# Performance work log

Measured on AMD Instinct MI355X. Metric: run time of the kernel, lower is better.

The kernel has to match this reference:

```python
import jax, jax.numpy as jnp
import numpy as np

B, S, DIM, H = 1, 4096, 1024, 16
HEAD_DIM = DIM // H
ROPE_THETA = 10000.0
LN_EPS = 1e-5


def _rope_cos_sin(seq_len, dim, theta):
    # frequencies over the FULL model dim (rope applied before head split, as in source)
    inv_freq = 1.0 / (theta ** (jnp.arange(0, dim, 2, dtype=jnp.float32) / dim))  # (dim/2,)
    ang = jnp.arange(seq_len, dtype=jnp.float32)[:, None] * inv_freq[None, :]     # (S, dim/2)
    cos = jnp.concatenate([jnp.cos(ang), jnp.cos(ang)], axis=-1)                  # (S, dim)
    sin = jnp.concatenate([jnp.sin(ang), jnp.sin(ang)], axis=-1)
    return cos, sin


def _rotate_half(x):
    d = x.shape[-1] // 2
    return jnp.concatenate([-x[..., d:], x[..., :d]], axis=-1)


def _apply_rope(x, cos, sin):
    # x: (B, S, dim); cos/sin: (S, dim)
    return x * cos[None] + _rotate_half(x) * sin[None]


def setup_inputs() -> dict:
    key = jax.random.key(0)
    ks = jax.random.split(key, 5)
    sc = 1.0 / np.sqrt(DIM)
    return {
        "x": jax.random.normal(ks[0], (B, S, DIM), dtype=jnp.float32),
        "Wqkv": jax.random.normal(ks[1], (DIM, 3 * DIM), dtype=jnp.float32) * sc,
        "bqkv": jax.random.normal(ks[2], (3 * DIM,), dtype=jnp.float32) * 0.01,
        "Wo": jax.random.normal(ks[3], (DIM, DIM), dtype=jnp.float32) * sc,
        "bo": jax.random.normal(ks[4], (DIM,), dtype=jnp.float32) * 0.01,
        "gamma": jnp.ones((DIM,), dtype=jnp.float32),
        "beta": jnp.zeros((DIM,), dtype=jnp.float32),
    }


def reference(x, Wqkv, bqkv, Wo, bo, gamma, beta):
    b, s, d = x.shape
    qkv = x @ Wqkv + bqkv                      # (B, S, 3*dim)
    q, k, v = jnp.split(qkv, 3, axis=-1)       # each (B, S, dim)
    cos, sin = _rope_cos_sin(s, d, ROPE_THETA)
    q = _apply_rope(q, cos, sin)
    k = _apply_rope(k, cos, sin)
    # split heads
    q = q.reshape(b, s, H, HEAD_DIM)
    k = k.reshape(b, s, H, HEAD_DIM)
    v = v.reshape(b, s, H, HEAD_DIM)
    scale = 1.0 / np.sqrt(HEAD_DIM)
    scores = jnp.einsum('bqhd,bkhd->bhqk', q, k) * scale  # (B, H, S, S)
    causal = jnp.triu(jnp.ones((s, s), dtype=bool), k=1)
    scores = jnp.where(causal[None, None], -jnp.inf, scores)
    attn = jax.nn.softmax(scores, axis=-1)
    out = jnp.einsum('bhqk,bkhd->bqhd', attn, v).reshape(b, s, d)
    out = out @ Wo + bo
    # LayerNorm (dropout is identity in eval mode)
    mu = jnp.mean(out, axis=-1, keepdims=True)
    var = jnp.mean(jnp.square(out - mu), axis=-1, keepdims=True)
    return (out - mu) * jax.lax.rsqrt(var + LN_EPS) * gamma + beta
```

## Files before the change

kernel.cpp:

```cpp
#include <hip/hip_runtime.h>
#include <cstdint>
#include <cstddef>

#define S_LEN 4096
#define DIM   1024
#define NH    16
#define HD    64
#define QKV_N 3072

typedef __attribute__((ext_vector_type(8))) short short8;
typedef __attribute__((ext_vector_type(4))) float f32x4;
typedef __attribute__((ext_vector_type(4))) unsigned short ushort4v;
typedef __attribute__((ext_vector_type(2))) unsigned int uint2v;

__device__ inline unsigned short f2bf(float x) {
    unsigned int u = __builtin_bit_cast(unsigned int, x);
    u += 0x7fffu + ((u >> 16) & 1u);
    return (unsigned short)(u >> 16);
}
__device__ inline float bf2f(unsigned short u) {
    return __builtin_bit_cast(float, (unsigned int)u << 16);
}
__device__ inline unsigned int pack2_bf16_rh(float lo, float hi) {
    unsigned int a = __builtin_bit_cast(unsigned int, lo) + 0x8000u;
    unsigned int b = __builtin_bit_cast(unsigned int, hi) + 0x8000u;
    return __builtin_amdgcn_perm(b, a, 0x07060302u);
}

__device__ inline void gl_lds16(const void* g, void* l) {
    __builtin_amdgcn_global_load_lds(
        (const __attribute__((address_space(1))) void*)g,
        (__attribute__((address_space(3))) void*)l, 16, 0, 0);
}

template <bool BF16OUT>
__global__ __launch_bounds__(256) void gemm_mfma_kernel(
    const unsigned short* __restrict__ A,
    const unsigned short* __restrict__ Bt,
    const float* __restrict__ bias,
    void* __restrict__ Cv,
    int M, int N, int K)
{
    __shared__ unsigned short As[128 * 32];
    __shared__ unsigned short Bs[128 * 32];

    const int t    = threadIdx.x;
    const int w    = t >> 6;
    const int lane = t & 63;
    const int ln   = lane & 15;
    const int quad = lane >> 4;
    const int bm   = blockIdx.y * 128;
    const int bn   = blockIdx.x * 128;
    const int wm   = (w & 1) * 64;
    const int wn   = (w >> 1) * 64;

    f32x4 acc[4][4];
#pragma unroll
    for (int i = 0; i < 4; ++i)
#pragma unroll
        for (int j = 0; j < 4; ++j) acc[i][j] = (f32x4){0.f, 0.f, 0.f, 0.f};

    const int lr = lane >> 2;
    const int lc = (lane & 3) * 8;
    const unsigned short* ga = A  + (size_t)(bm + w * 32 + lr) * K + lc;
    const unsigned short* gb = Bt + (size_t)(bn + w * 32 + lr) * K + lc;
    unsigned short* la = &As[(w * 32) * 32];
    unsigned short* lb = &Bs[(w * 32) * 32];

    for (int k0 = 0; k0 < K; k0 += 32) {
        gl_lds16(ga,            la);
        gl_lds16(ga + 16 * K,   la + 16 * 32);
        gl_lds16(gb,            lb);
        gl_lds16(gb + 16 * K,   lb + 16 * 32);
        ga += 32; gb += 32;
        __syncthreads();

        short8 af[4], bf[4];
#pragma unroll
        for (int i = 0; i < 4; ++i)
            af[i] = *(const short8*)&As[(wm + i * 16 + ln) * 32 + quad * 8];
#pragma unroll
        for (int j = 0; j < 4; ++j)
            bf[j] = *(const short8*)&Bs[(wn + j * 16 + ln) * 32 + quad * 8];
#pragma unroll
        for (int i = 0; i < 4; ++i)
#pragma unroll
            for (int j = 0; j < 4; ++j)
                acc[i][j] = __builtin_amdgcn_mfma_f32_16x16x32_bf16(af[i], bf[j], acc[i][j], 0, 0, 0);
        __syncthreads();
    }

#pragma unroll
    for (int j = 0; j < 4; ++j) {
        const int col = bn + wn + j * 16 + ln;
        const float bv = bias[col];
#pragma unroll
        for (int i = 0; i < 4; ++i) {
            const int row0 = bm + wm + i * 16 + quad * 4;
#pragma unroll
            for (int r = 0; r < 4; ++r) {
                const float v = acc[i][j][r] + bv;
                if (BF16OUT)
                    ((unsigned short*)Cv)[(size_t)(row0 + r) * N + col] = f2bf(v);
                else
                    ((float*)Cv)[(size_t)(row0 + r) * N + col] = v;
            }
        }
    }
}

__global__ __launch_bounds__(256) void prep1_kernel(
    const float* __restrict__ x, unsigned short* __restrict__ xb,
    const float* __restrict__ Wqkv, unsigned short* __restrict__ WqkvT,
    const float* __restrict__ Wo, unsigned short* __restrict__ WoT)
{
    __shared__ unsigned short L[64][72];
    const int b = blockIdx.x;
    const int t = threadIdx.x;

    if (b < 2048) {
        const size_t i = ((size_t)b * 256 + t) * 8;
        float4 a = *(const float4*)(x + i);
        float4 c = *(const float4*)(x + i + 4);
        short8 p = { (short)f2bf(a.x), (short)f2bf(a.y), (short)f2bf(a.z), (short)f2bf(a.w),
                     (short)f2bf(c.x), (short)f2bf(c.y), (short)f2bf(c.z), (short)f2bf(c.w) };
        *(short8*)(xb + i) = p;
        return;
    }
    const float* W;
    unsigned short* Wt;
    int N, n0, k0;
    if (b < 2816) {
        const int wb = b - 2048;
        W = Wqkv; Wt = WqkvT; N = QKV_N;
        n0 = (wb % 48) * 64; k0 = (wb / 48) * 64;
    } else {
        const int wb = b - 2816;
        W = Wo; Wt = WoT; N = DIM;
        n0 = (wb & 15) * 64; k0 = (wb >> 4) * 64;
    }
    const int kr = t >> 2, cb = (t & 3) * 16;
    const float* wp = W + (size_t)(k0 + kr) * N + n0 + cb;
#pragma unroll
    for (int u = 0; u < 16; u += 4) {
        float4 v = *(const float4*)(wp + u);
        ushort4v p = { f2bf(v.x), f2bf(v.y), f2bf(v.z), f2bf(v.w) };
        *(ushort4v*)&L[kr][cb + u] = p;
    }
    __syncthreads();
    const int nr = t >> 2, kb = (t & 3) * 16;
    short8 lo, hi;
#pragma unroll
    for (int u = 0; u < 8; ++u) lo[u] = (short)L[kb + u][nr];
#pragma unroll
    for (int u = 0; u < 8; ++u) hi[u] = (short)L[kb + 8 + u][nr];
    unsigned short* op = Wt + (size_t)(n0 + nr) * 1024 + k0 + kb;
    *(short8*)op       = lo;
    *(short8*)(op + 8) = hi;
}

__global__ __launch_bounds__(256) void prep2_kernel(
    const unsigned short* __restrict__ qkvb,
    unsigned short* __restrict__ Qb,
    unsigned short* __restrict__ Kb,
    unsigned short* __restrict__ Vt)
{
    __shared__ unsigned short L[64][72];
    const int b = blockIdx.x;
    const int t = threadIdx.x;

    if (b < 2048) {
        const int idx = b * 256 + t;
        const int j   = (idx & 127) * 4;
        const int s   = idx >> 7;
        const unsigned short* row = qkvb + (size_t)s * QKV_N;
        unsigned short* qo = Qb + (size_t)s * DIM;
        unsigned short* ko = Kb + (size_t)s * DIM;
        const float sf = (float)s;
        const float QSCALE = 0.18033688011112042f;
        const float C1 = -0.025952563241307517f;
        const float INV2PI = 0.15915494309189535f;

        float cs[4], sn[4];
#pragma unroll
        for (int e = 0; e < 4; ++e) {
            const float invf2pi = exp2f((float)(j + e) * C1) * INV2PI;
            float rev = sf * invf2pi;
            rev -= floorf(rev);
            sn[e] = __builtin_amdgcn_sinf(rev);
            cs[e] = __builtin_amdgcn_cosf(rev);
        }
        ushort4v q1 = *(const ushort4v*)(row + j);
        ushort4v q2 = *(const ushort4v*)(row + 512 + j);
        ushort4v k1 = *(const ushort4v*)(row + DIM + j);
        ushort4v k2 = *(const ushort4v*)(row + DIM + 512 + j);
        ushort4v qa, qb4, ka, kb4;
#pragma unroll
        for (int e = 0; e < 4; ++e) {
            const float x1 = bf2f(q1[e]), x2 = bf2f(q2[e]);
            const float y1 = bf2f(k1[e]), y2 = bf2f(k2[e]);
            qa[e]  = f2bf((x1 * cs[e] - x2 * sn[e]) * QSCALE);
            qb4[e] = f2bf((x2 * cs[e] + x1 * sn[e]) * QSCALE);
            ka[e]  = f2bf(y1 * cs[e] - y2 * sn[e]);
            kb4[e] = f2bf(y2 * cs[e] + y1 * sn[e]);
        }
        *(ushort4v*)(qo + j)       = qa;
        *(ushort4v*)(qo + 512 + j) = qb4;
        *(ushort4v*)(ko + j)       = ka;
        *(ushort4v*)(ko + 512 + j) = kb4;
        return;
    }

    const int vb = b - 2048;
    const int c0 = (vb & 15) * 64;
    const int bs = (vb >> 4) * 64;
    const int sl = t >> 2, cb = (t & 3) * 16;
    const unsigned short* vp = qkvb + (size_t)(bs + sl) * QKV_N + 2 * DIM + c0 + cb;
    *(short8*)&L[sl][cb]     = *(const short8*)vp;
    *(short8*)&L[sl][cb + 8] = *(const short8*)(vp + 8);
    __syncthreads();
    const int cl = t >> 2, sb = (t & 3) * 16;
    short8 lo, hi;
#pragma unroll
    for (int u = 0; u < 8; ++u) lo[u] = (short)L[sb + u][cl];
#pragma unroll
    for (int u = 0; u < 8; ++u) hi[u] = (short)L[sb + 8 + u][cl];
    unsigned short* op = Vt + (size_t)(c0 + cl) * S_LEN + bs + sb;
    *(short8*)op       = lo;
    *(short8*)(op + 8) = hi;
}

__global__ __launch_bounds__(256) void attn_mfma_kernel(
    const unsigned short* __restrict__ Qb,
    const unsigned short* __restrict__ Kb,
    const unsigned short* __restrict__ Vt,
    float* __restrict__ Op,
    float* __restrict__ lp)
{
    __shared__ unsigned short Ks[64][72];
    __shared__ unsigned short Vs[64][72];
    __shared__ unsigned short Ps[4][16][72];

    const int t    = threadIdx.x;
    const int w    = t >> 6;
    const int lane = t & 63;
    const int ln   = lane & 15;
    const int quad = lane >> 4;
    const int p    = blockIdx.x;
    const int half = blockIdx.y;
    const int h    = blockIdx.z;

    const int sc_ = t >> 2;
    const int so  = (t & 3) * 16;

#pragma unroll
    for (int phase = 0; phase < 2; ++phase) {
        const int qt  = phase == 0 ? (63 - p) : p;
        const int q0  = qt * 64;
        const int nkt = qt + 1;
        const int c0  = (nkt + 1) >> 1;
        const int kt_begin = half == 0 ? 0 : c0;
        const int kt_end   = half == 0 ? c0 : nkt;

        short8 qf[2];
        {
            const unsigned short* qp = Qb + (size_t)(q0 + w * 16 + ln) * DIM + h * HD + quad * 8;
            qf[0] = *(const short8*)qp;
            qf[1] = *(const short8*)(qp + 32);
        }

        f32x4 o[4];
#pragma unroll
        for (int db = 0; db < 4; ++db) o[db] = (f32x4){0.f, 0.f, 0.f, 0.f};
        float lrow = 0.f;

        short8 kr0, kr1, vr0, vr1;
        {
            const int k0 = kt_begin * 64;
            const unsigned short* kp = Kb + (size_t)(k0 + sc_) * DIM + h * HD + so;
            kr0 = *(const short8*)kp;  kr1 = *(const short8*)(kp + 8);
            const unsigned short* vp = Vt + (size_t)(h * HD + sc_) * S_LEN + k0 + so;
            vr0 = *(const short8*)vp;  vr1 = *(const short8*)(vp + 8);
        }

        for (int kt = kt_begin; kt < kt_end; ++kt) {
            __syncthreads();
            *(short8*)&Ks[sc_][so]     = kr0;
            *(short8*)&Ks[sc_][so + 8] = kr1;
            *(short8*)&Vs[sc_][so]     = vr0;
            *(short8*)&Vs[sc_][so + 8] = vr1;
            if (kt + 1 < kt_end) {
                const int k1 = (kt + 1) * 64;
                const unsigned short* kp = Kb + (size_t)(k1 + sc_) * DIM + h * HD + so;
                kr0 = *(const short8*)kp;  kr1 = *(const short8*)(kp + 8);
                const unsigned short* vp = Vt + (size_t)(h * HD + sc_) * S_LEN + k1 + so;
                vr0 = *(const short8*)vp;  vr1 = *(const short8*)(vp + 8);
            }
            __syncthreads();

            f32x4 sc[4];
#pragma unroll
            for (int kb = 0; kb < 4; ++kb) sc[kb] = (f32x4){0.f, 0.f, 0.f, 0.f};
#pragma unroll
            for (int kk = 0; kk < 2; ++kk) {
#pragma unroll
                for (int kb = 0; kb < 4; ++kb) {
                    short8 kf = *(const short8*)&Ks[kb * 16 + ln][kk * 32 + quad * 8];
                    sc[kb] = __builtin_amdgcn_mfma_f32_16x16x32_bf16(kf, qf[kk], sc[kb], 0, 0, 0);
                }
            }

            if (kt == nkt - 1) {
                const int qg = w * 16 + ln;
                const int kb0 = kt * 64 - q0;
#pragma unroll
                for (int kb = 0; kb < 4; ++kb) {
                    const int key = kb0 + kb * 16 + quad * 4;
#pragma unroll
                    for (int r = 0; r < 4; ++r)
                        if (key + r > qg) sc[kb][r] = -1e30f;
                }
            }

            float psp[4];
#pragma unroll
            for (int kb = 0; kb < 4; ++kb) {
                float pv[4];
#pragma unroll
                for (int r = 0; r < 4; ++r) pv[r] = exp2f(sc[kb][r]);
                psp[kb] = (pv[0] + pv[1]) + (pv[2] + pv[3]);
                uint2v pk = { pack2_bf16_rh(pv[0], pv[1]), pack2_bf16_rh(pv[2], pv[3]) };
                *(uint2v*)&Ps[w][ln][kb * 16 + quad * 4] = pk;
            }
            float ps = (psp[0] + psp[1]) + (psp[2] + psp[3]);
            ps += __shfl_xor(ps, 16);
            ps += __shfl_xor(ps, 32);
            lrow += ps;

#pragma unroll
            for (int kk = 0; kk < 2; ++kk) {
                short8 pf = *(const short8*)&Ps[w][ln][kk * 32 + quad * 8];
#pragma unroll
                for (int db = 0; db < 4; ++db) {
                    short8 vf = *(const short8*)&Vs[db * 16 + ln][kk * 32 + quad * 8];
                    o[db] = __builtin_amdgcn_mfma_f32_16x16x32_bf16(vf, pf, o[db], 0, 0, 0);
                }
            }
        }

        {
            float* op = Op + ((size_t)half * S_LEN + q0 + w * 16 + ln) * DIM + h * HD + quad * 4;
#pragma unroll
            for (int db = 0; db < 4; ++db)
                *(f32x4*)(op + db * 16) = o[db];
            if (quad == 0)
                lp[((size_t)half * NH + h) * S_LEN + q0 + w * 16 + ln] = lrow;
        }
    }
}

__global__ __launch_bounds__(256) void combine_kernel(
    const float* __restrict__ Op, const float* __restrict__ lp,
    unsigned short* __restrict__ attnb)
{
    const int row = blockIdx.x;
    const int t   = threadIdx.x;
    const int d   = t * 4;
    const int h   = t >> 4;
    f32x4 a = *(const f32x4*)&Op[(size_t)row * DIM + d];
    f32x4 b = *(const f32x4*)&Op[((size_t)S_LEN + row) * DIM + d];
    const float l = lp[(size_t)h * S_LEN + row] + lp[((size_t)NH + h) * S_LEN + row];
    const float inv = 1.0f / l;
    ushort4v o;
#pragma unroll
    for (int e = 0; e < 4; ++e) o[e] = f2bf((a[e] + b[e]) * inv);
    *(ushort4v*)&attnb[(size_t)row * DIM + d] = o;
}

__global__ __launch_bounds__(256) void ln_kernel(
    const float* __restrict__ in, const float* __restrict__ gamma,
    const float* __restrict__ beta, float* __restrict__ out)
{
    const int row = blockIdx.x;
    const int t = threadIdx.x;
    const float4 v = *(const float4*)&in[(size_t)row * DIM + t * 4];
    float s  = v.x + v.y + v.z + v.w;
    float sq = v.x * v.x + v.y * v.y + v.z * v.z + v.w * v.w;
#pragma unroll
    for (int off = 1; off < 64; off <<= 1) {
        s  += __shfl_xor(s, off);
        sq += __shfl_xor(sq, off);
    }
    __shared__ float red[8];
    const int wv = t >> 6, ln = t & 63;
    if (ln == 0) { red[wv] = s; red[4 + wv] = sq; }
    __syncthreads();
    s  = red[0] + red[1] + red[2] + red[3];
    sq = red[4] + red[5] + red[6] + red[7];
    const float mu  = s * (1.0f / DIM);
    const float var = sq * (1.0f / DIM) - mu * mu;
    const float rs  = rsqrtf(var + 1e-5f);
    const float4 g = *(const float4*)&gamma[t * 4];
    const float4 b = *(const float4*)&beta[t * 4];
    float4 o = { (v.x - mu) * rs * g.x + b.x,
                 (v.y - mu) * rs * g.y + b.y,
                 (v.z - mu) * rs * g.z + b.z,
                 (v.w - mu) * rs * g.w + b.w };
    *(float4*)&out[(size_t)row * DIM + t * 4] = o;
}

extern "C" void kernel_launch(void* const* d_in, const int* in_sizes, int n_in,
                              void* d_out, int out_size, void* d_ws, size_t ws_size,
                              hipStream_t stream)
{
    const float* x     = (const float*)d_in[0];
    const float* Wqkv  = (const float*)d_in[1];
    const float* bqkv  = (const float*)d_in[2];
    const float* Wo    = (const float*)d_in[3];
    const float* bo    = (const float*)d_in[4];
    const float* gamma = (const float*)d_in[5];
    const float* beta  = (const float*)d_in[6];
    float* out = (float*)d_out;

    char* base = (char*)d_ws;
    unsigned short* qkvb  = (unsigned short*)base;
    unsigned short* attnb = (unsigned short*)base;
    float* Op   = (float*)(base + (size_t)8 * 1024 * 1024);
    float* proj = (float*)(base + (size_t)8 * 1024 * 1024);
    float* lp   = (float*)(base + (size_t)40 * 1024 * 1024);
    unsigned short* Qb    = (unsigned short*)(base + (size_t)48 * 1024 * 1024);
    unsigned short* Kb    = (unsigned short*)(base + (size_t)56 * 1024 * 1024);
    unsigned short* Vt    = (unsigned short*)(base + (size_t)64 * 1024 * 1024);
    unsigned short* xb    = (unsigned short*)(base + (size_t)72 * 1024 * 1024);
    unsigned short* WqkvT = (unsigned short*)(base + (size_t)80 * 1024 * 1024);
    unsigned short* WoT   = (unsigned short*)(base + (size_t)86 * 1024 * 1024);

    prep1_kernel<<<3072, 256, 0, stream>>>(x, xb, Wqkv, WqkvT, Wo, WoT);

    gemm_mfma_kernel<true><<<dim3(QKV_N / 128, S_LEN / 128), 256, 0, stream>>>(
        xb, WqkvT, bqkv, qkvb, S_LEN, QKV_N, DIM);

    prep2_kernel<<<3072, 256, 0, stream>>>(qkvb, Qb, Kb, Vt);

    attn_mfma_kernel<<<dim3(32, 2, NH), 256, 0, stream>>>(Qb, Kb, Vt, Op, lp);

    combine_kernel<<<S_LEN, 256, 0, stream>>>(Op, lp, attnb);

    gemm_mfma_kernel<false><<<dim3(DIM / 128, S_LEN / 128), 256, 0, stream>>>(
        attnb, WoT, bo, proj, S_LEN, DIM, DIM);

    ln_kernel<<<S_LEN, 256, 0, stream>>>(proj, gamma, beta, out);
}
```

Measured before the change: 259.9 us.

## Rework attention to 32x32 MFMA tiles with register-resident P and swizzled LDS

The attention kernel moves from 16x16x32 to 32x32x16 bf16 MFMA, with each wave owning 32 query rows, so a block now covers 128 queries and the grid halves. The softmax probabilities stay in registers and are rearranged with v_permlane32_swap instead of a round trip through shared memory. K and V tiles are double-buffered in XOR-swizzled LDS, which drops one barrier per iteration and avoids bank conflicts. The trade-offs are higher register pressure, fewer blocks to balance the causal work, and a wider causal-mask region spanning two key tiles.

```diff
diff --git a/kernel.cpp b/kernel.cpp
--- a/kernel.cpp
+++ b/kernel.cpp
@@ -10,8 +10,10 @@
 
 typedef __attribute__((ext_vector_type(8))) short short8;
 typedef __attribute__((ext_vector_type(4))) float f32x4;
+typedef __attribute__((ext_vector_type(16))) float f32x16;
 typedef __attribute__((ext_vector_type(4))) unsigned short ushort4v;
 typedef __attribute__((ext_vector_type(2))) unsigned int uint2v;
+typedef __attribute__((ext_vector_type(4))) unsigned int uint4v;
 
 __device__ inline unsigned short f2bf(float x) {
     unsigned int u = __builtin_bit_cast(unsigned int, x);
@@ -237,124 +239,144 @@
     float* __restrict__ Op,
     float* __restrict__ lp)
 {
-    __shared__ unsigned short Ks[64][72];
-    __shared__ unsigned short Vs[64][72];
-    __shared__ unsigned short Ps[4][16][72];
+    __shared__ unsigned short Ks[2][64 * 64];
+    __shared__ unsigned short Vs[2][64 * 64];
 
     const int t    = threadIdx.x;
     const int w    = t >> 6;
     const int lane = t & 63;
-    const int ln   = lane & 15;
-    const int quad = lane >> 4;
+    const int r31  = lane & 31;
+    const int hi   = lane >> 5;
     const int p    = blockIdx.x;
     const int half = blockIdx.y;
     const int h    = blockIdx.z;
 
-    const int sc_ = t >> 2;
-    const int so  = (t & 3) * 16;
+    const int srow  = t >> 2;
+    const int sch   = (t & 3) * 2;
+    const int ssw   = srow & 7;
+    const int soff0 = srow * 64 + ((sch ^ ssw) << 3);
+    const int soff1 = srow * 64 + (((sch + 1) ^ ssw) << 3);
+
+    const int rA = r31 * 64;
+    const int sw = r31 & 7;
 
 #pragma unroll
     for (int phase = 0; phase < 2; ++phase) {
-        const int qt  = phase == 0 ? (63 - p) : p;
-        const int q0  = qt * 64;
-        const int nkt = qt + 1;
-        const int c0  = (nkt + 1) >> 1;
+        const int qt  = phase == 0 ? (31 - p) : p;
+        const int q0  = qt * 128;
+        const int nkt = 2 * qt + 2;
+        const int c0  = nkt >> 1;
         const int kt_begin = half == 0 ? 0 : c0;
         const int kt_end   = half == 0 ? c0 : nkt;
 
-        short8 qf[2];
+        short8 qf[4];
         {
-            const unsigned short* qp = Qb + (size_t)(q0 + w * 16 + ln) * DIM + h * HD + quad * 8;
-            qf[0] = *(const short8*)qp;
-            qf[1] = *(const short8*)(qp + 32);
-        }
-
-        f32x4 o[4];
-#pragma unroll
-        for (int db = 0; db < 4; ++db) o[db] = (f32x4){0.f, 0.f, 0.f, 0.f};
+            const unsigned short* qp = Qb + (size_t)(q0 + w * 32 + r31) * DIM + h * HD + hi * 8;
+#pragma unroll
+            for (int kk = 0; kk < 4; ++kk) qf[kk] = *(const short8*)(qp + kk * 16);
+        }
+
+        f32x16 o0 = {}, o1 = {};
         float lrow = 0.f;
 
         short8 kr0, kr1, vr0, vr1;
         {
             const int k0 = kt_begin * 64;
-            const unsigned short* kp = Kb + (size_t)(k0 + sc_) * DIM + h * HD + so;
+            const unsigned short* kp = Kb + (size_t)(k0 + srow) * DIM + h * HD + sch * 8;
             kr0 = *(const short8*)kp;  kr1 = *(const short8*)(kp + 8);
-            const unsigned short* vp = Vt + (size_t)(h * HD + sc_) * S_LEN + k0 + so;
+            const unsigned short* vp = Vt + (size_t)(h * HD + srow) * S_LEN + k0 + sch * 8;
             vr0 = *(const short8*)vp;  vr1 = *(const short8*)(vp + 8);
         }
+        __syncthreads();
 
         for (int kt = kt_begin; kt < kt_end; ++kt) {
-            __syncthreads();
-            *(short8*)&Ks[sc_][so]     = kr0;
-            *(short8*)&Ks[sc_][so + 8] = kr1;
-            *(short8*)&Vs[sc_][so]     = vr0;
-            *(short8*)&Vs[sc_][so + 8] = vr1;
+            const int buf = (kt - kt_begin) & 1;
+            unsigned short* ks = &Ks[buf][0];
+            unsigned short* vs = &Vs[buf][0];
+            *(short8*)&ks[soff0] = kr0;
+            *(short8*)&ks[soff1] = kr1;
+            *(short8*)&vs[soff0] = vr0;
+            *(short8*)&vs[soff1] = vr1;
             if (kt + 1 < kt_end) {
                 const int k1 = (kt + 1) * 64;
-                const unsigned short* kp = Kb + (size_t)(k1 + sc_) * DIM + h * HD + so;
+                const unsigned short* kp = Kb + (size_t)(k1 + srow) * DIM + h * HD + sch * 8;
                 kr0 = *(const short8*)kp;  kr1 = *(const short8*)(kp + 8);
-                const unsigned short* vp = Vt + (size_t)(h * HD + sc_) * S_LEN + k1 + so;
+                const unsigned short* vp = Vt + (size_t)(h * HD + srow) * S_LEN + k1 + sch * 8;
                 vr0 = *(const short8*)vp;  vr1 = *(const short8*)(vp + 8);
             }
             __syncthreads();
 
-            f32x4 sc[4];
-#pragma unroll
-            for (int kb = 0; kb < 4; ++kb) sc[kb] = (f32x4){0.f, 0.f, 0.f, 0.f};
-#pragma unroll
-            for (int kk = 0; kk < 2; ++kk) {
-#pragma unroll
-                for (int kb = 0; kb < 4; ++kb) {
-                    short8 kf = *(const short8*)&Ks[kb * 16 + ln][kk * 32 + quad * 8];
-                    sc[kb] = __builtin_amdgcn_mfma_f32_16x16x32_bf16(kf, qf[kk], sc[kb], 0, 0, 0);
-                }
-            }
-
-            if (kt == nkt - 1) {
-                const int qg = w * 16 + ln;
-                const int kb0 = kt * 64 - q0;
-#pragma unroll
-                for (int kb = 0; kb < 4; ++kb) {
-                    const int key = kb0 + kb * 16 + quad * 4;
-#pragma unroll
-                    for (int r = 0; r < 4; ++r)
-                        if (key + r > qg) sc[kb][r] = -1e30f;
-                }
-            }
-
-            float psp[4];
-#pragma unroll
-            for (int kb = 0; kb < 4; ++kb) {
-                float pv[4];
-#pragma unroll
-                for (int r = 0; r < 4; ++r) pv[r] = exp2f(sc[kb][r]);
-                psp[kb] = (pv[0] + pv[1]) + (pv[2] + pv[3]);
-                uint2v pk = { pack2_bf16_rh(pv[0], pv[1]), pack2_bf16_rh(pv[2], pv[3]) };
-                *(uint2v*)&Ps[w][ln][kb * 16 + quad * 4] = pk;
-            }
-            float ps = (psp[0] + psp[1]) + (psp[2] + psp[3]);
-            ps += __shfl_xor(ps, 16);
+            f32x16 s0 = {}, s1 = {};
+#pragma unroll
+            for (int kk = 0; kk < 4; ++kk) {
+                const int co = (((kk * 2 + hi) ^ sw) << 3);
+                short8 kf0 = *(const short8*)&ks[rA + co];
+                short8 kf1 = *(const short8*)&ks[rA + 2048 + co];
+                s0 = __builtin_amdgcn_mfma_f32_32x32x16_bf16(kf0, qf[kk], s0, 0, 0, 0);
+                s1 = __builtin_amdgcn_mfma_f32_32x32x16_bf16(kf1, qf[kk], s1, 0, 0, 0);
+            }
+
+            if (kt >= nkt - 2) {
+                const int qg = q0 + w * 32 + r31;
+                const int kb = kt * 64 + 4 * hi;
+#pragma unroll
+                for (int g = 0; g < 4; ++g)
+#pragma unroll
+                    for (int a = 0; a < 4; ++a) {
+                        const int keyl = kb + a + 8 * g;
+                        if (keyl > qg)      s0[4 * g + a] = -1e30f;
+                        if (keyl + 32 > qg) s1[4 * g + a] = -1e30f;
+                    }
+            }
+
+            unsigned int pd0[8], pd1[8];
+            float ps = 0.f;
+#pragma unroll
+            for (int g = 0; g < 4; ++g) {
+                const float a0 = exp2f(s0[4 * g + 0]), a1 = exp2f(s0[4 * g + 1]);
+                const float a2 = exp2f(s0[4 * g + 2]), a3 = exp2f(s0[4 * g + 3]);
+                const float b0 = exp2f(s1[4 * g + 0]), b1 = exp2f(s1[4 * g + 1]);
+                const float b2 = exp2f(s1[4 * g + 2]), b3 = exp2f(s1[4 * g + 3]);
+                ps += ((a0 + a1) + (a2 + a3)) + ((b0 + b1) + (b2 + b3));
+                pd0[2 * g]     = pack2_bf16_rh(a0, a1);
+                pd0[2 * g + 1] = pack2_bf16_rh(a2, a3);
+                pd1[2 * g]     = pack2_bf16_rh(b0, b1);
+                pd1[2 * g + 1] = pack2_bf16_rh(b2, b3);
+            }
             ps += __shfl_xor(ps, 32);
             lrow += ps;
 
 #pragma unroll
-            for (int kk = 0; kk < 2; ++kk) {
-                short8 pf = *(const short8*)&Ps[w][ln][kk * 32 + quad * 8];
-#pragma unroll
-                for (int db = 0; db < 4; ++db) {
-                    short8 vf = *(const short8*)&Vs[db * 16 + ln][kk * 32 + quad * 8];
-                    o[db] = __builtin_amdgcn_mfma_f32_16x16x32_bf16(vf, pf, o[db], 0, 0, 0);
-                }
+            for (int w16 = 0; w16 < 4; ++w16) {
+                const int lw = w16 & 1;
+                unsigned int a0, b0, a1, b1;
+                if (w16 < 2) { a0 = pd0[4 * lw];     b0 = pd0[4 * lw + 2];
+                               a1 = pd0[4 * lw + 1]; b1 = pd0[4 * lw + 3]; }
+                else         { a0 = pd1[4 * lw];     b0 = pd1[4 * lw + 2];
+                               a1 = pd1[4 * lw + 1]; b1 = pd1[4 * lw + 3]; }
+                asm("v_permlane32_swap_b32 %0, %1" : "+v"(a0), "+v"(b0));
+                asm("v_permlane32_swap_b32 %0, %1" : "+v"(a1), "+v"(b1));
+                const uint4v frw = { a0, a1, b0, b1 };
+                const short8 pf = __builtin_bit_cast(short8, frw);
+                const int co = (((w16 * 2 + hi) ^ sw) << 3);
+                short8 vf0 = *(const short8*)&vs[rA + co];
+                short8 vf1 = *(const short8*)&vs[rA + 2048 + co];
+                o0 = __builtin_amdgcn_mfma_f32_32x32x16_bf16(vf0, pf, o0, 0, 0, 0);
+                o1 = __builtin_amdgcn_mfma_f32_32x32x16_bf16(vf1, pf, o1, 0, 0, 0);
             }
         }
 
         {
-            float* op = Op + ((size_t)half * S_LEN + q0 + w * 16 + ln) * DIM + h * HD + quad * 4;
-#pragma unroll
-            for (int db = 0; db < 4; ++db)
-                *(f32x4*)(op + db * 16) = o[db];
-            if (quad == 0)
-                lp[((size_t)half * NH + h) * S_LEN + q0 + w * 16 + ln] = lrow;
+            float* op = Op + ((size_t)half * S_LEN + q0 + w * 32 + r31) * DIM + h * HD + hi * 4;
+#pragma unroll
+            for (int g = 0; g < 4; ++g) {
+                f32x4 v0 = { o0[4 * g + 0], o0[4 * g + 1], o0[4 * g + 2], o0[4 * g + 3] };
+                f32x4 v1 = { o1[4 * g + 0], o1[4 * g + 1], o1[4 * g + 2], o1[4 * g + 3] };
+                *(f32x4*)(op + g * 8)      = v0;
+                *(f32x4*)(op + 32 + g * 8) = v1;
+            }
+            if (hi == 0)
+                lp[((size_t)half * NH + h) * S_LEN + q0 + w * 32 + r31] = lrow;
         }
     }
 }
@@ -442,7 +464,7 @@
 
     prep2_kernel<<<3072, 256, 0, stream>>>(qkvb, Qb, Kb, Vt);
 
-    attn_mfma_kernel<<<dim3(32, 2, NH), 256, 0, stream>>>(Qb, Kb, Vt, Op, lp);
+    attn_mfma_kernel<<<dim3(16, 2, NH), 256, 0, stream>>>(Qb, Kb, Vt, Op, lp);
 
     combine_kernel<<<S_LEN, 256, 0, stream>>>(Op, lp, attnb);
 
```

Result: faster. 248.6 us (-4.3%).
